# Performance work log

Hardware: AMD Instinct MI355X
Metric: run time of the kernel (lower is better)

The kernel has to match this reference:

```python
import jax, jax.numpy as jnp
import numpy as np

H = 768          # hidden_size
NH = 12          # num_attention_heads
DH = H // NH     # attention_head_size = 64
NE_TYPES = 16    # num_edge_types
B, S = 4, 512
N = B * S        # flattened node count
E = 131072       # number of edges


def setup_inputs() -> dict:
    key = jax.random.key(0)
    ks = jax.random.split(key, 12)
    inp = {
        "hidden_states": jax.random.normal(ks[0], (B, S, H), dtype=jnp.float32),
        "Wq": jax.random.normal(ks[1], (H, H), dtype=jnp.float32) * 0.02,
        "bq": jnp.zeros((H,), dtype=jnp.float32),
        "Wk": jax.random.normal(ks[2], (H, H), dtype=jnp.float32) * 0.02,
        "bk": jnp.zeros((H,), dtype=jnp.float32),
        "Wv": jax.random.normal(ks[3], (H, H), dtype=jnp.float32) * 0.02,
        "bv": jnp.zeros((H,), dtype=jnp.float32),
        "rel_key_emb": jax.random.normal(ks[4], (NE_TYPES, DH), dtype=jnp.float32) * 0.02,
        "rel_val_emb": jax.random.normal(ks[5], (NE_TYPES, DH), dtype=jnp.float32) * 0.02,
        "edges_src": jax.random.randint(ks[6], (E,), 0, N, dtype=jnp.int32),
        "edges_tgt": jax.random.randint(ks[7], (E,), 0, N, dtype=jnp.int32),
        "edges_type": jax.random.randint(ks[8], (E,), 0, NE_TYPES, dtype=jnp.int32),
        "edges_pos": jax.random.randint(ks[9], (E,), 0, NE_TYPES, dtype=jnp.int32),
    }
    return inp


def reference(hidden_states, Wq, bq, Wk, bk, Wv, bv, rel_key_emb, rel_val_emb,
              edges_src, edges_tgt, edges_type, edges_pos):
    b, s, h = hidden_states.shape
    n = b * s
    hs = hidden_states.reshape(n, h)
    # Q/K/V projections, split into heads: [N, NH, DH]
    q = (hs @ Wq.T + bq).reshape(n, NH, DH)
    k = (hs @ Wk.T + bk).reshape(n, NH, DH)
    v = (hs @ Wv.T + bv).reshape(n, NH, DH)
    # Edge gather + relative key embedding (broadcast over heads)
    src_key = k[edges_src] + rel_key_emb[edges_pos][:, None, :]      # [E, NH, DH]
    tgt_query = q[edges_tgt]                                          # [E, NH, DH]
    # Unnormalized exp attention scores per edge per head: [E, NH]
    scores = jnp.exp(jnp.sum(tgt_query * src_key, axis=-1) / jnp.sqrt(jnp.float32(DH)))
    # Segment softmax normalization via scatter-add over target nodes
    denom = jax.ops.segment_sum(scores, edges_tgt, num_segments=n)    # [N, NH]
    attn = scores / denom[edges_tgt]                                  # [E, NH]
    # Reweighted per-edge values (the meaningful computed quantity)
    src_val = v[edges_src] + rel_val_emb[edges_pos][:, None, :]       # [E, NH, DH]
    weighted = src_val * attn[:, :, None]                             # [E, NH, DH]
    # NOTE: the original torch forward returns hidden_states unchanged
    # (the attention chain is dead code). We return the computed edge-weighted
    # values as the correctness target for the gather->exp->scatter-softmax chain.
    return weighted
```

## Files before the change

### kernel.cpp

```cpp
#include <hip/hip_runtime.h>
#include <hip/hip_bf16.h>

#define H 768
#define NH 12
#define DH 64
#define NNODES 2048
#define NEDGES 131072

typedef __bf16 bf16x8 __attribute__((ext_vector_type(8)));
typedef float floatx4 __attribute__((ext_vector_type(4)));

__global__ __launch_bounds__(256)
void convert_kernel(const float* __restrict__ hs,
                    const float* __restrict__ Wq,
                    const float* __restrict__ Wk,
                    const float* __restrict__ Wv,
                    __hip_bfloat16* __restrict__ hsb,
                    __hip_bfloat16* __restrict__ wb) {
  int i = blockIdx.x * 256 + threadIdx.x;
  const int n_hs = NNODES * H;
  const int n_w  = H * H;
  if (i < n_hs) {
    hsb[i] = __float2bfloat16(hs[i]);
    return;
  }
  int j = i - n_hs;
  if (j < 3 * n_w) {
    const float* src = (j < n_w) ? Wq : (j < 2 * n_w ? Wk : Wv);
    wb[j] = __float2bfloat16(src[j % n_w]);
  }
}

__global__ __launch_bounds__(256)
void qkv_gemm(const __hip_bfloat16* __restrict__ A,
              const __hip_bfloat16* __restrict__ Wb,
              const float* __restrict__ b0,
              const float* __restrict__ b1,
              const float* __restrict__ b2,
              float* __restrict__ out) {
  __shared__ __hip_bfloat16 As[128][32];
  __shared__ __hip_bfloat16 Bs[128][32];

  const int t    = threadIdx.x;
  const int wave = t >> 6;
  const int lane = t & 63;
  const int bm   = blockIdx.x * 128;
  const int bn   = blockIdx.y * 128;
  const int mat  = blockIdx.z;

  const __hip_bfloat16* B = Wb + (size_t)mat * H * H;
  const float* bias = (mat == 0) ? b0 : ((mat == 1) ? b1 : b2);
  float* C = out + (size_t)mat * NNODES * H;

  const int wm = (wave & 1) * 64;
  const int wn = (wave >> 1) * 64;
  const int lr = lane & 15;
  const int lq = lane >> 4;

  floatx4 acc[4][4] = {};

  const int ar = t >> 2;
  const int ac = (t & 3) * 8;

  for (int kt = 0; kt < H; kt += 32) {
    uint4 va0 = *(const uint4*)(A + (size_t)(bm + ar) * H + kt + ac);
    uint4 va1 = *(const uint4*)(A + (size_t)(bm + 64 + ar) * H + kt + ac);
    uint4 vb0 = *(const uint4*)(B + (size_t)(bn + ar) * H + kt + ac);
    uint4 vb1 = *(const uint4*)(B + (size_t)(bn + 64 + ar) * H + kt + ac);
    *(uint4*)&As[ar][ac]      = va0;
    *(uint4*)&As[64 + ar][ac] = va1;
    *(uint4*)&Bs[ar][ac]      = vb0;
    *(uint4*)&Bs[64 + ar][ac] = vb1;
    __syncthreads();

    bf16x8 af[4], bfr[4];
#pragma unroll
    for (int i = 0; i < 4; i++)
      af[i] = *(const bf16x8*)&As[wm + i * 16 + lr][lq * 8];
#pragma unroll
    for (int i = 0; i < 4; i++)
      bfr[i] = *(const bf16x8*)&Bs[wn + i * 16 + lr][lq * 8];
#pragma unroll
    for (int mi = 0; mi < 4; mi++)
#pragma unroll
      for (int ni = 0; ni < 4; ni++)
        acc[mi][ni] = __builtin_amdgcn_mfma_f32_16x16x32_bf16(
            af[mi], bfr[ni], acc[mi][ni], 0, 0, 0);
    __syncthreads();
  }

#pragma unroll
  for (int ni = 0; ni < 4; ni++) {
    int col = bn + wn + ni * 16 + lr;
    float bv = bias[col];
#pragma unroll
    for (int mi = 0; mi < 4; mi++) {
#pragma unroll
      for (int r = 0; r < 4; r++) {
        int row = bm + wm + mi * 16 + lq * 4 + r;
        C[(size_t)row * H + col] = acc[mi][ni][r] + bv;
      }
    }
  }
}

__global__ __launch_bounds__(256)
void zero_kernel(float* __restrict__ p, int n) {
  int i = blockIdx.x * 256 + threadIdx.x;
  if (i < n) p[i] = 0.0f;
}

__global__ __launch_bounds__(256)
void scores_kernel(const float* __restrict__ Q, const float* __restrict__ K,
                   const float* __restrict__ relk,
                   const int* __restrict__ esrc, const int* __restrict__ etgt,
                   const int* __restrict__ epos,
                   float* __restrict__ scores, float* __restrict__ denom) {
  const int wave = threadIdx.x >> 6;
  const int lane = threadIdx.x & 63;
  const int e = blockIdx.x * 4 + wave;
  const int src = esrc[e], tgt = etgt[e], pos = epos[e];
  const int g = lane >> 4;
  const int off = (lane & 15) * 4;

  const float4 r4 = *(const float4*)(relk + pos * DH + off);
  float s[3];
#pragma unroll
  for (int c = 0; c < 3; c++) {
    const float4 q4 = *(const float4*)(Q + (size_t)tgt * H + c * 256 + lane * 4);
    const float4 k4 = *(const float4*)(K + (size_t)src * H + c * 256 + lane * 4);
    s[c] = q4.x * (k4.x + r4.x) + q4.y * (k4.y + r4.y) +
           q4.z * (k4.z + r4.z) + q4.w * (k4.w + r4.w);
  }
#pragma unroll
  for (int m = 1; m < 16; m <<= 1) {
    s[0] += __shfl_xor(s[0], m);
    s[1] += __shfl_xor(s[1], m);
    s[2] += __shfl_xor(s[2], m);
  }
  if ((lane & 15) == 0) {
#pragma unroll
    for (int c = 0; c < 3; c++) {
      float sc = __expf(s[c] * 0.125f);
      int h = c * 4 + g;
      scores[(size_t)e * NH + h] = sc;
      atomicAdd(denom + (size_t)tgt * NH + h, sc);
    }
  }
}

__global__ __launch_bounds__(256)
void weighted_kernel(const float* __restrict__ V, const float* __restrict__ relv,
                     const int* __restrict__ esrc, const int* __restrict__ etgt,
                     const int* __restrict__ epos,
                     const float* __restrict__ scores,
                     const float* __restrict__ denom,
                     float* __restrict__ out) {
  const int wave = threadIdx.x >> 6;
  const int lane = threadIdx.x & 63;
  const int e = blockIdx.x * 4 + wave;
  const int src = esrc[e], tgt = etgt[e], pos = epos[e];
  const int g = lane >> 4;
  const int off = (lane & 15) * 4;

  const float4 r4 = *(const float4*)(relv + pos * DH + off);
#pragma unroll
  for (int c = 0; c < 3; c++) {
    int h = c * 4 + g;
    float a = scores[(size_t)e * NH + h] / denom[(size_t)tgt * NH + h];
    float4 v4 = *(const float4*)(V + (size_t)src * H + c * 256 + lane * 4);
    float4 o;
    o.x = (v4.x + r4.x) * a;
    o.y = (v4.y + r4.y) * a;
    o.z = (v4.z + r4.z) * a;
    o.w = (v4.w + r4.w) * a;
    *(float4*)(out + (size_t)e * H + c * 256 + lane * 4) = o;
  }
}

extern "C" void kernel_launch(void* const* d_in, const int* in_sizes, int n_in,
                              void* d_out, int out_size, void* d_ws, size_t ws_size,
                              hipStream_t stream) {
  const float* hs   = (const float*)d_in[0];
  const float* Wq   = (const float*)d_in[1];
  const float* bq   = (const float*)d_in[2];
  const float* Wk   = (const float*)d_in[3];
  const float* bk   = (const float*)d_in[4];
  const float* Wv   = (const float*)d_in[5];
  const float* bv   = (const float*)d_in[6];
  const float* relk = (const float*)d_in[7];
  const float* relv = (const float*)d_in[8];
  const int* esrc   = (const int*)d_in[9];
  const int* etgt   = (const int*)d_in[10];
  const int* epos   = (const int*)d_in[12];
  float* out = (float*)d_out;

  char* ws = (char*)d_ws;
  __hip_bfloat16* hsb = (__hip_bfloat16*)ws;
  __hip_bfloat16* wb  = (__hip_bfloat16*)(ws + 3145728);
  float* qkv    = (float*)(ws + 6684672);
  float* scores = (float*)(ws + 25559040);
  float* denom  = (float*)(ws + 31850496);

  convert_kernel<<<13056, 256, 0, stream>>>(hs, Wq, Wk, Wv, hsb, wb);

  dim3 grid_gemm(16, 6, 3);
  qkv_gemm<<<grid_gemm, 256, 0, stream>>>(hsb, wb, bq, bk, bv, qkv);

  zero_kernel<<<96, 256, 0, stream>>>(denom, NNODES * NH);

  const float* Qp = qkv;
  const float* Kp = qkv + (size_t)NNODES * H;
  const float* Vp = qkv + (size_t)2 * NNODES * H;

  scores_kernel<<<NEDGES / 4, 256, 0, stream>>>(Qp, Kp, relk, esrc, etgt, epos,
                                                scores, denom);

  weighted_kernel<<<NEDGES / 4, 256, 0, stream>>>(Vp, relv, esrc, etgt, epos,
                                                  scores, denom, out);
}
```

Before: 573.4 us.

## Vectorize conversion, fuse denom zeroing, use direct LDS loads and nontemporal stores

The fp32-to-bf16 conversion now processes four elements per thread and also zeroes the softmax denominator, which removes the separate zero kernel launch. The GEMM tile loads use global_load_lds to write global data straight into LDS without passing through registers. The large per-edge output is written with nontemporal stores to reduce cache pollution. These are several independent memory-path tweaks, and the direct-LDS loads depend on gfx950 support for 16-byte transfers.

```diff
diff --git a/kernel.cpp b/kernel.cpp
--- a/kernel.cpp
+++ b/kernel.cpp
@@ -10,24 +10,43 @@
 typedef __bf16 bf16x8 __attribute__((ext_vector_type(8)));
 typedef float floatx4 __attribute__((ext_vector_type(4)));
 
+#define GLOAD_LDS16(gptr, ldsptr)                                                        \
+  __builtin_amdgcn_global_load_lds((const __attribute__((address_space(1))) void*)(gptr), \
+                                   (__attribute__((address_space(3))) void*)(ldsptr),     \
+                                   16, 0, 0)
+
+__device__ __forceinline__ unsigned short f2bf(float x) {
+  union { __hip_bfloat16 h; unsigned short u; } cv;
+  cv.h = __float2bfloat16(x);
+  return cv.u;
+}
+
 __global__ __launch_bounds__(256)
 void convert_kernel(const float* __restrict__ hs,
                     const float* __restrict__ Wq,
                     const float* __restrict__ Wk,
                     const float* __restrict__ Wv,
                     __hip_bfloat16* __restrict__ hsb,
-                    __hip_bfloat16* __restrict__ wb) {
+                    __hip_bfloat16* __restrict__ wb,
+                    float* __restrict__ denom) {
   int i = blockIdx.x * 256 + threadIdx.x;
-  const int n_hs = NNODES * H;
-  const int n_w  = H * H;
-  if (i < n_hs) {
-    hsb[i] = __float2bfloat16(hs[i]);
+  const int n_hs4 = NNODES * H / 4;
+  const int n_w4  = H * H / 4;
+  if (i < n_hs4) {
+    float4 v = ((const float4*)hs)[i];
+    ((ushort4*)hsb)[i] = make_ushort4(f2bf(v.x), f2bf(v.y), f2bf(v.z), f2bf(v.w));
     return;
   }
-  int j = i - n_hs;
-  if (j < 3 * n_w) {
-    const float* src = (j < n_w) ? Wq : (j < 2 * n_w ? Wk : Wv);
-    wb[j] = __float2bfloat16(src[j % n_w]);
+  int j = i - n_hs4;
+  if (j < 3 * n_w4) {
+    const float* src = (j < n_w4) ? Wq : (j < 2 * n_w4 ? Wk : Wv);
+    float4 v = ((const float4*)src)[j % n_w4];
+    ((ushort4*)wb)[j] = make_ushort4(f2bf(v.x), f2bf(v.y), f2bf(v.z), f2bf(v.w));
+    return;
+  }
+  int z = j - 3 * n_w4;
+  if (z < NNODES * NH / 4) {
+    ((float4*)denom)[z] = make_float4(0.f, 0.f, 0.f, 0.f);
   }
 }
 
@@ -61,16 +80,14 @@
 
   const int ar = t >> 2;
   const int ac = (t & 3) * 8;
+  __hip_bfloat16* AsF = &As[0][0];
+  __hip_bfloat16* BsF = &Bs[0][0];
 
   for (int kt = 0; kt < H; kt += 32) {
-    uint4 va0 = *(const uint4*)(A + (size_t)(bm + ar) * H + kt + ac);
-    uint4 va1 = *(const uint4*)(A + (size_t)(bm + 64 + ar) * H + kt + ac);
-    uint4 vb0 = *(const uint4*)(B + (size_t)(bn + ar) * H + kt + ac);
-    uint4 vb1 = *(const uint4*)(B + (size_t)(bn + 64 + ar) * H + kt + ac);
-    *(uint4*)&As[ar][ac]      = va0;
-    *(uint4*)&As[64 + ar][ac] = va1;
-    *(uint4*)&Bs[ar][ac]      = vb0;
-    *(uint4*)&Bs[64 + ar][ac] = vb1;
+    GLOAD_LDS16(A + (size_t)(bm + ar) * H + kt + ac,      AsF + t * 8);
+    GLOAD_LDS16(A + (size_t)(bm + 64 + ar) * H + kt + ac, AsF + 64 * 32 + t * 8);
+    GLOAD_LDS16(B + (size_t)(bn + ar) * H + kt + ac,      BsF + t * 8);
+    GLOAD_LDS16(B + (size_t)(bn + 64 + ar) * H + kt + ac, BsF + 64 * 32 + t * 8);
     __syncthreads();
 
     bf16x8 af[4], bfr[4];
@@ -102,12 +119,6 @@
       }
     }
   }
-}
-
-__global__ __launch_bounds__(256)
-void zero_kernel(float* __restrict__ p, int n) {
-  int i = blockIdx.x * 256 + threadIdx.x;
-  if (i < n) p[i] = 0.0f;
 }
 
 __global__ __launch_bounds__(256)
@@ -169,12 +180,12 @@
     int h = c * 4 + g;
     float a = scores[(size_t)e * NH + h] / denom[(size_t)tgt * NH + h];
     float4 v4 = *(const float4*)(V + (size_t)src * H + c * 256 + lane * 4);
-    float4 o;
+    floatx4 o;
     o.x = (v4.x + r4.x) * a;
     o.y = (v4.y + r4.y) * a;
     o.z = (v4.z + r4.z) * a;
     o.w = (v4.w + r4.w) * a;
-    *(float4*)(out + (size_t)e * H + c * 256 + lane * 4) = o;
+    __builtin_nontemporal_store(o, (floatx4*)(out + (size_t)e * H + c * 256 + lane * 4));
   }
 }
 
@@ -202,12 +213,10 @@
   float* scores = (float*)(ws + 25559040);
   float* denom  = (float*)(ws + 31850496);
 
-  convert_kernel<<<13056, 256, 0, stream>>>(hs, Wq, Wk, Wv, hsb, wb);
+  convert_kernel<<<3288, 256, 0, stream>>>(hs, Wq, Wk, Wv, hsb, wb, denom);
 
   dim3 grid_gemm(16, 6, 3);
   qkv_gemm<<<grid_gemm, 256, 0, stream>>>(hsb, wb, bq, bk, bv, qkv);
-
-  zero_kernel<<<96, 256, 0, stream>>>(denom, NNODES * NH);
 
   const float* Qp = qkv;
   const float* Kp = qkv + (size_t)NNODES * H;
```

Result: faster. 539.8 us (-5.9%).
